# Kernel optimization log

Measured on AMD Instinct MI355X. Metric: run time of the kernel, lower is better.

The kernel has to match this reference:

```python
import jax, jax.numpy as jnp
import numpy as np

N_NODES = 50000
N_EDGES = 1600000
IN_DIM = 128
OUT_DIM = 128
NEG_SLOPE = 0.01  # torch F.leaky_relu default


def setup_inputs() -> dict:
    key = jax.random.key(0)
    ks = jax.random.split(key, 8)
    feat = jax.random.normal(ks[0], (N_NODES, IN_DIM), dtype=jnp.float32)
    src = jax.random.randint(ks[1], (N_EDGES,), 0, N_NODES, dtype=jnp.int32)
    dst = jax.random.randint(ks[2], (N_EDGES,), 0, N_NODES, dtype=jnp.int32)
    W = jax.random.normal(ks[3], (IN_DIM, OUT_DIM), dtype=jnp.float32) / np.sqrt(IN_DIM)
    b = jax.random.normal(ks[4], (OUT_DIM,), dtype=jnp.float32) * 0.01
    attn_w = jax.random.normal(ks[5], (2 * OUT_DIM, 1), dtype=jnp.float32) / np.sqrt(2 * OUT_DIM)
    attn_b = jax.random.normal(ks[6], (1,), dtype=jnp.float32) * 0.01
    mask_weights = jnp.ones((IN_DIM,), dtype=jnp.float32)
    return {"feat": feat, "src": src, "dst": dst, "W": W, "b": b,
            "attn_w": attn_w, "attn_b": attn_b, "mask_weights": mask_weights}


def reference(feat, src, dst, W, b, attn_w, attn_b, mask_weights):
    N = feat.shape[0]
    d = W.shape[1]
    # feature masking + linear projection: [N, out_dim]
    h = (feat * jax.nn.sigmoid(mask_weights)) @ W + b
    # edge scores: attn_mlp(cat([h_src, h_dst])) split into two GEMVs to avoid
    # materializing the [E, 2d] concat
    s_src = (h @ attn_w[:d]).squeeze(-1)   # [N]
    s_dst = (h @ attn_w[d:]).squeeze(-1)   # [N]
    score = s_src[src] + s_dst[dst] + attn_b[0]          # [E]
    score = jnp.where(score >= 0, score, NEG_SLOPE * score)  # leaky_relu
    # segment softmax grouped by destination node (dgl.softmax over in-edges)
    mx = jax.ops.segment_max(score, dst, num_segments=N)     # [N]
    mx = jnp.where(jnp.isfinite(mx), mx, 0.0)                 # nodes w/o edges
    ex = jnp.exp(score - mx[dst])                             # [E]
    denom = jax.ops.segment_sum(ex, dst, num_segments=N)     # [N]
    a = ex / jnp.where(denom == 0, 1.0, denom)[dst]           # [E]
    # weighted scatter-sum: h_new[v] = sum_{(u,v) in E} a_uv * h[u]
    h_new = jax.ops.segment_sum(h[src] * a[:, None], dst, num_segments=N)
    return h_new
```

## Files before the change

kernel.cpp:

```cpp
#include <hip/hip_runtime.h>
#include <hip/hip_fp16.h>
#include <math.h>

#define N_NODES 50000
#define N_EDGES 1600000
#define NB 2000
#define NPB 25
#define NCH 100
#define EPC 16000
#define CAPC 32
#define CAP_LDS 1280
#define CAP_STG 1080
#define RCAP 96
#define SPLIT 8
#define BPS (NB / SPLIT)
#define PLACE_BLOCKS (NCH * SPLIT)
#define PROJ_BLOCKS ((N_NODES + 31) / 32)
#define NBG 5
#define NGRP (NBG * NPB)
#define GQ_BLOCKS ((NB / (NBG * 2)) * 8)

typedef _Float16 f16x8 __attribute__((ext_vector_type(8)));
typedef float f32x4 __attribute__((ext_vector_type(4)));


__global__ __launch_bounds__(256) void k_prep(const float* __restrict__ W,
                                              const float* __restrict__ b,
                                              const float* __restrict__ attn_w,
                                              __half* __restrict__ w16q,
                                              float* __restrict__ waSD,
                                              float* __restrict__ cst) {
    const int blk = blockIdx.x, t = threadIdx.x;
    if (blk < 8) {
        const int k = blk * 16 + (t >> 4), sub = t & 15;
        const float4* W4 = (const float4*)W;
        float4 w0 = W4[k * 32 + sub * 2];
        float4 w1 = W4[k * 32 + sub * 2 + 1];
        const int j0 = sub * 8;
        float pS = w0.x * attn_w[j0]     + w0.y * attn_w[j0 + 1]
                 + w0.z * attn_w[j0 + 2] + w0.w * attn_w[j0 + 3]
                 + w1.x * attn_w[j0 + 4] + w1.y * attn_w[j0 + 5]
                 + w1.z * attn_w[j0 + 6] + w1.w * attn_w[j0 + 7];
        float pD = w0.x * attn_w[128 + j0]     + w0.y * attn_w[128 + j0 + 1]
                 + w0.z * attn_w[128 + j0 + 2] + w0.w * attn_w[128 + j0 + 3]
                 + w1.x * attn_w[128 + j0 + 4] + w1.y * attn_w[128 + j0 + 5]
                 + w1.z * attn_w[128 + j0 + 6] + w1.w * attn_w[128 + j0 + 7];
        pS += __shfl_down(pS, 8); pS += __shfl_down(pS, 4);
        pS += __shfl_down(pS, 2); pS += __shfl_down(pS, 1);
        pD += __shfl_down(pD, 8); pD += __shfl_down(pD, 4);
        pD += __shfl_down(pD, 2); pD += __shfl_down(pD, 1);
        if (sub == 0) { waSD[k] = pS; waSD[128 + k] = pD; }
    } else if (blk < 40) {
        for (int e = (blk - 8) * 256 + t; e < 16384; e += 8192) {
            int j = e & 7, l = (e >> 3) & 63, kb = (e >> 9) & 3, ct = e >> 11;
            int k = kb * 32 + (l >> 4) * 8 + j;
            int c = ct * 16 + (l & 15);
            w16q[e] = __float2half(W[k * 128 + c]);
        }
    } else if (t < 64) {
        float vS = b[t] * attn_w[t]       + b[t + 64] * attn_w[t + 64];
        float vD = b[t] * attn_w[128 + t] + b[t + 64] * attn_w[192 + t];
        for (int off = 32; off; off >>= 1) {
            vS += __shfl_down(vS, off);
            vD += __shfl_down(vD, off);
        }
        if (t == 0) { cst[0] = vS; cst[1] = vD; }
    }
}

__global__ __launch_bounds__(512) void k_fusedA(const float* __restrict__ feat,
                                                const float* __restrict__ b,
                                                const float* __restrict__ mask,
                                                const int* __restrict__ src,
                                                const int* __restrict__ dst,
                                                __half* __restrict__ h16q,
                                                float* __restrict__ s_src,
                                                float* __restrict__ s_dst,
                                                int* __restrict__ cnt,
                                                unsigned* __restrict__ gep,
                                                const __half* __restrict__ w16q,
                                                const float* __restrict__ waSD,
                                                const float* __restrict__ cst) {
    __shared__ __align__(16) char smem[33024];
    const int blk = blockIdx.x;
    const int t = threadIdx.x;

    if (blk < PLACE_BLOCKS) {
        int* cur = (int*)smem;
        unsigned* lcell = (unsigned*)(smem + 1024);
        const int c = blk >> 3, sp = blk & 7;
        const int b0 = sp * BPS;
        for (int i = t; i < BPS; i += 512) cur[i] = 0;
        __syncthreads();
        const int q0 = c * (EPC / 4);
        for (int q = t; q < EPC / 4; q += 512) {
            int4 s4 = ((const int4*)src)[q0 + q];
            int4 d4 = ((const int4*)dst)[q0 + q];
            int ss[4] = {s4.x, s4.y, s4.z, s4.w};
            int dd[4] = {d4.x, d4.y, d4.z, d4.w};
#pragma unroll
            for (int k = 0; k < 4; k++) {
                int d = dd[k];
                int bkt = d / NPB;
                if (bkt >= b0 && bkt < b0 + BPS) {
                    int dl = d - bkt * NPB;
                    int lb = bkt - b0;
                    int r = atomicAdd(&cur[lb], 1);
                    if (r < CAPC)
                        lcell[lb * CAPC + r] = ((unsigned)ss[k] << 5) | (unsigned)dl;
                }
            }
        }
        __syncthreads();
        const uint4* lc4 = (const uint4*)lcell;
        uint4* gp4 = (uint4*)gep;
        for (int idx = t; idx < BPS * (CAPC / 4); idx += 512) {
            int i = idx >> 3, q = idx & 7;
            gp4[((size_t)(b0 + i) * NCH + c) * 8 + q] = lc4[idx];
        }
        for (int i = t; i < BPS; i += 512)
            cnt[(b0 + i) * NCH + c] = min(cur[i], CAPC);
    } else {
        float* sAW = (float*)(smem + 8192);
        float* sAD = (float*)(smem + 8704);
        float* sig = (float*)(smem + 9216);
        const int bb = blk - PLACE_BLOCKS;
        const int row0 = bb * 32;
        if (t < 128) {
            sig[t] = 1.f / (1.f + expf(-mask[t]));
            sAW[t] = waSD[t];
            sAD[t] = waSD[128 + t];
        }
        __syncthreads();
        for (int idx = t; idx < 32 * 32; idx += 512) {
            int r = idx >> 5, c4 = idx & 31;
            int grow = row0 + r;
            float4 f;
            if (grow < N_NODES) f = ((const float4*)feat)[grow * 32 + c4];
            else f = make_float4(0.f, 0.f, 0.f, 0.f);
            int c = c4 * 4;
            ushort4 pk;
            pk.x = __half_as_ushort(__float2half(f.x * sig[c]));
            pk.y = __half_as_ushort(__float2half(f.y * sig[c + 1]));
            pk.z = __half_as_ushort(__float2half(f.z * sig[c + 2]));
            pk.w = __half_as_ushort(__float2half(f.w * sig[c + 3]));
            int byte = (r * 256 + c4 * 8) ^ ((r & 7) << 4);
            *(ushort4*)(smem + byte) = pk;
        }
        __syncthreads();
        const int wv = t >> 6, l = t & 63;
        const int lr = l & 15, lk = l >> 4;
        const f16x8* wq = (const f16x8*)w16q;
        f32x4 acc0 = {0.f, 0.f, 0.f, 0.f};
        f32x4 acc1 = {0.f, 0.f, 0.f, 0.f};
#pragma unroll
        for (int kb = 0; kb < 4; kb++) {
            f16x8 Bf = wq[(wv * 4 + kb) * 64 + l];
            int co = kb * 64 + lk * 16;
            f16x8 A0 = *(const f16x8*)(smem + ((lr * 256 + co) ^ ((lr & 7) << 4)));
            f16x8 A1 = *(const f16x8*)(smem + (((16 + lr) * 256 + co) ^ ((lr & 7) << 4)));
            acc0 = __builtin_amdgcn_mfma_f32_16x16x32_f16(A0, Bf, acc0, 0, 0, 0);
            acc1 = __builtin_amdgcn_mfma_f32_16x16x32_f16(A1, Bf, acc1, 0, 0, 0);
        }
        {
            const int r2 = t >> 4, sub = t & 15;
            f16x8 xv = *(const f16x8*)(smem + ((r2 * 256 + sub * 16) ^ ((r2 & 7) << 4)));
            float ss = 0.f, sd = 0.f;
#pragma unroll
            for (int q = 0; q < 8; q++) {
                float v = (float)xv[q];
                int jj = sub * 8 + q;
                ss = fmaf(v, sAW[jj], ss);
                sd = fmaf(v, sAD[jj], sd);
            }
            ss += __shfl_down(ss, 8); ss += __shfl_down(ss, 4);
            ss += __shfl_down(ss, 2); ss += __shfl_down(ss, 1);
            sd += __shfl_down(sd, 8); sd += __shfl_down(sd, 4);
            sd += __shfl_down(sd, 2); sd += __shfl_down(sd, 1);
            int grow = row0 + r2;
            if (sub == 0 && grow < N_NODES) {
                s_src[grow] = ss + cst[0];
                s_dst[grow] = sd + cst[1];
            }
        }
        const float bj = b[wv * 16 + lr];
        __half* hp = h16q + (size_t)(wv >> 1) * (N_NODES * 32) + ((wv & 1) * 16 + lr);
#pragma unroll
        for (int reg = 0; reg < 4; reg++) {
            int n0 = row0 + lk * 4 + reg;
            if (n0 < N_NODES) hp[(size_t)n0 * 32] = __float2half(acc0[reg] + bj);
            int n1 = n0 + 16;
            if (n1 < N_NODES) hp[(size_t)n1 * 32] = __float2half(acc1[reg] + bj);
        }
    }
}

__global__ __launch_bounds__(256) void k_sort(const float* __restrict__ s_src,
                                              const float* __restrict__ s_dst,
                                              const float* __restrict__ attn_b,
                                              const int* __restrict__ cnt,
                                              unsigned* gep,
                                              int* __restrict__ rp_g) {
    __shared__ unsigned raw[CAP_STG];
    __shared__ unsigned srt[CAP_LDS];
    __shared__ float wbuf[CAP_LDS];
    __shared__ int ccnt[NCH];
    __shared__ int coff[NCH];
    __shared__ int hist[NPB];
    __shared__ int rp[NPB + 1];
    __shared__ float sdl[NPB];
    __shared__ float dinv[NPB];
    __shared__ int totsh;
    const int bkt = blockIdx.x;
    const int t = threadIdx.x;
    if (t < NCH) ccnt[t] = cnt[bkt * NCH + t];
    if (t < NPB) { hist[t] = 0; sdl[t] = s_dst[bkt * NPB + t]; }
    __syncthreads();
    if (t < 64) {
        int i0 = 2 * t, i1 = 2 * t + 1;
        int a0 = (i0 < NCH) ? ccnt[i0] : 0;
        int a1 = (i1 < NCH) ? ccnt[i1] : 0;
        int s = a0 + a1, incl = s;
#pragma unroll
        for (int off = 1; off < 64; off <<= 1) {
            int v = __shfl_up(incl, off);
            if (t >= off) incl += v;
        }
        int excl = incl - s;
        if (i0 < NCH) coff[i0] = excl;
        if (i1 < NCH) coff[i1] = excl + a0;
        if (t == 63) totsh = incl;
    }
    __syncthreads();
    int total = totsh;
    if (total > CAP_STG) total = CAP_STG;
    unsigned* gb = gep + (size_t)bkt * (NCH * CAPC);
    for (int i = t; i < NCH * CAPC; i += 256) {
        unsigned e = gb[i];
        int cell = i >> 5, slot = i & 31;
        if (slot < ccnt[cell]) {
            int pos = coff[cell] + slot;
            if (pos < CAP_STG) {
                int r = atomicAdd(&hist[e & 31], 1);
                raw[pos] = ((unsigned)r << 21) | e;
            }
        }
    }
    __syncthreads();
    if (t < 64) {
        int h = (t < NPB) ? min(hist[t], RCAP) : 0;
        int incl = h;
#pragma unroll
        for (int off = 1; off < 32; off <<= 1) {
            int v = __shfl_up(incl, off);
            if (t >= off) incl += v;
        }
        if (t < NPB) rp[t] = incl - h;
        if (t == NPB - 1) rp[NPB] = incl;
    }
    __syncthreads();
    const float ab = attn_b[0];
    {
        unsigned ev[5];
        float ssv[5];
#pragma unroll
        for (int k = 0; k < 5; k++) {
            int i = t + k * 256;
            ev[k] = (i < total) ? raw[i] : 0xFFFFFFFFu;
        }
#pragma unroll
        for (int k = 0; k < 5; k++)
            ssv[k] = s_src[(ev[k] != 0xFFFFFFFFu) ? (int)((ev[k] >> 5) & 0xFFFFu) : 0];
#pragma unroll
        for (int k = 0; k < 5; k++) {
            if (ev[k] != 0xFFFFFFFFu) {
                unsigned e = ev[k];
                int dl = (int)(e & 31);
                int r = (int)((e >> 21) & 0x7FF);
                if (r < RCAP) {
                    int pos = rp[dl] + r;
                    float sc = ssv[k] + sdl[dl] + ab;
                    sc = sc >= 0.f ? sc : 0.01f * sc;
                    float w = __expf(sc);
                    srt[pos] = (((e >> 5) & 0xFFFFu) << 16) | (unsigned)dl;
                    wbuf[pos] = w;
                }
            }
        }
    }
    __syncthreads();
    if (t < NPB * 8) {
        const int n = t >> 3, sub = t & 7;
        const int lo = rp[n], hi = rp[n + 1];
        float s = 0.f;
        for (int i = lo + sub; i < hi; i += 8) s += wbuf[i];
        s += __shfl_down(s, 4); s += __shfl_down(s, 2); s += __shfl_down(s, 1);
        if (sub == 0) dinv[n] = s > 0.f ? 1.f / s : 0.f;
    }
    __syncthreads();
    const int totp = rp[NPB];
    for (int i = t; i < totp; i += 256) {
        unsigned e = srt[i];
        float a = wbuf[i] * dinv[e & 31];
        gb[i] = (e & 0xFFFF0000u) | (unsigned)__half_as_ushort(__float2half(a));
    }
    if (t <= NPB) rp_g[bkt * 32 + t] = rp[t];
}

__device__ __forceinline__ void accum8(float4& A, float4& B, uint4 u, unsigned e) {
    float w = __half2float(__ushort_as_half((unsigned short)(e & 0xFFFFu)));
    __half2 p0 = *(const __half2*)&u.x;
    __half2 p1 = *(const __half2*)&u.y;
    __half2 p2 = *(const __half2*)&u.z;
    __half2 p3 = *(const __half2*)&u.w;
    float2 f0 = __half22float2(p0), f1 = __half22float2(p1);
    float2 f2 = __half22float2(p2), f3 = __half22float2(p3);
    A.x = fmaf(w, f0.x, A.x); A.y = fmaf(w, f0.y, A.y);
    A.z = fmaf(w, f1.x, A.z); A.w = fmaf(w, f1.y, A.w);
    B.x = fmaf(w, f2.x, B.x); B.y = fmaf(w, f2.y, B.y);
    B.z = fmaf(w, f3.x, B.z); B.w = fmaf(w, f3.y, B.w);
}

__global__ __launch_bounds__(512) void k_gather(const __half* __restrict__ h16q,
                                                const unsigned* __restrict__ gep,
                                                const int* __restrict__ rp_g,
                                                float* __restrict__ out) {
    __shared__ unsigned se[NBG * CAP_LDS];
    __shared__ int rp[NBG * 32];
    const int blk = blockIdx.x;
    const int x = blk & 7;
    const int qq = x & 3;
    const int bg = ((blk >> 3) << 1) + (x >> 2);
    const int bkt0 = bg * NBG;
    const int t = threadIdx.x;
    if (t < NBG * 32 && (t & 31) <= NPB)
        rp[t] = rp_g[(bkt0 + (t >> 5)) * 32 + (t & 31)];
    __syncthreads();
#pragma unroll
    for (int b = 0; b < NBG; b++) {
        const unsigned* gb = gep + (size_t)(bkt0 + b) * (NCH * CAPC);
        const int tot = rp[b * 32 + NPB];
        for (int i = t; i < tot; i += 512) se[b * CAP_LDS + i] = gb[i];
    }
    __syncthreads();
    const int g = t >> 2, dp = t & 3;
    if (g < NGRP) {
        const int b = g / NPB, n = g - b * NPB;
        const int lo = rp[b * 32 + n], hi = rp[b * 32 + n + 1];
        const unsigned* seb = se + b * CAP_LDS;
        const uint4* hq = (const uint4*)h16q + (size_t)qq * (N_NODES * 4) + dp;
        float4 A = {0.f, 0.f, 0.f, 0.f}, B = {0.f, 0.f, 0.f, 0.f};
        for (int i = lo; i < hi; i += 4) {
            unsigned e0 = seb[i];
            unsigned e1 = (i + 1 < hi) ? seb[i + 1] : 0u;
            unsigned e2 = (i + 2 < hi) ? seb[i + 2] : 0u;
            unsigned e3 = (i + 3 < hi) ? seb[i + 3] : 0u;
            uint4 u0 = hq[(e0 >> 16) * 4];
            uint4 u1 = hq[(e1 >> 16) * 4];
            uint4 u2 = hq[(e2 >> 16) * 4];
            uint4 u3 = hq[(e3 >> 16) * 4];
            accum8(A, B, u0, e0);
            accum8(A, B, u1, e1);
            accum8(A, B, u2, e2);
            accum8(A, B, u3, e3);
        }
        float4* o = (float4*)(out + (size_t)(bg * 125 + g) * 128 + qq * 32 + dp * 8);
        o[0] = A;
        o[1] = B;
    }
}

extern "C" void kernel_launch(void* const* d_in, const int* in_sizes, int n_in,
                              void* d_out, int out_size, void* d_ws, size_t ws_size,
                              hipStream_t stream) {
    const float* feat   = (const float*)d_in[0];
    const int*   src    = (const int*)d_in[1];
    const int*   dst    = (const int*)d_in[2];
    const float* W      = (const float*)d_in[3];
    const float* b      = (const float*)d_in[4];
    const float* attn_w = (const float*)d_in[5];
    const float* attn_b = (const float*)d_in[6];
    const float* mask   = (const float*)d_in[7];
    float* out = (float*)d_out;

    char* ws = (char*)d_ws;
    __half*   h16q  = (__half*)(ws + 0);
    float*    s_src = (float*)(ws + 12800000);
    float*    s_dst = (float*)(ws + 13000000);
    int*      cnt   = (int*)(ws + 13200000);
    unsigned* gep   = (unsigned*)(ws + 14000000);
    int*      rp_g  = (int*)(ws + 39600000);
    __half*   w16q  = (__half*)(ws + 39856000);
    float*    waSD  = (float*)(ws + 39888768);
    float*    cst   = (float*)(ws + 39889792);

    k_prep<<<41, 256, 0, stream>>>(W, b, attn_w, w16q, waSD, cst);
    k_fusedA<<<PLACE_BLOCKS + PROJ_BLOCKS, 512, 0, stream>>>(
        feat, b, mask, src, dst, h16q, s_src, s_dst, cnt, gep, w16q, waSD, cst);
    k_sort<<<NB, 256, 0, stream>>>(s_src, s_dst, attn_b, cnt, gep, rp_g);
    k_gather<<<GQ_BLOCKS, 512, 0, stream>>>(h16q, gep, rp_g, out);
}
```

Baseline: 173.3 us.

## Compact edge placement via global atomic bucket counters instead of padded chunk cells

Placement blocks now reserve space in each destination bucket with a global atomicAdd per bucket and write only the valid edges contiguously into a compact per-bucket array. Before, they wrote fixed 32-slot cells per chunk, and the sort kernel had to read all 3200 padded slots and prefix-sum the chunk counts. This cuts global write and read traffic for the edge buffer and simplifies the sort kernel. Block indexing is also remapped so that blocks handling different chunks run together, which spreads contention on the atomics. The cost is global atomic traffic, nondeterministic edge order within a bucket, and an extra pass in k_prep to zero the counters.

```diff
diff --git a/kernel.cpp b/kernel.cpp
--- a/kernel.cpp
+++ b/kernel.cpp
@@ -9,12 +9,12 @@
 #define NCH 100
 #define EPC 16000
 #define CAPC 32
-#define CAP_LDS 1280
 #define CAP_STG 1080
+#define GEPS 1088
 #define RCAP 96
 #define SPLIT 8
 #define BPS (NB / SPLIT)
-#define PLACE_BLOCKS (NCH * SPLIT)
+#define PLACE_EXT 832
 #define PROJ_BLOCKS ((N_NODES + 31) / 32)
 #define NBG 5
 #define NGRP (NBG * NPB)
@@ -29,7 +29,8 @@
                                               const float* __restrict__ attn_w,
                                               __half* __restrict__ w16q,
                                               float* __restrict__ waSD,
-                                              float* __restrict__ cst) {
+                                              float* __restrict__ cst,
+                                              int* __restrict__ gcnt) {
     const int blk = blockIdx.x, t = threadIdx.x;
     if (blk < 8) {
         const int k = blk * 16 + (t >> 4), sub = t & 15;
@@ -57,14 +58,19 @@
             int c = ct * 16 + (l & 15);
             w16q[e] = __float2half(W[k * 128 + c]);
         }
-    } else if (t < 64) {
-        float vS = b[t] * attn_w[t]       + b[t + 64] * attn_w[t + 64];
-        float vD = b[t] * attn_w[128 + t] + b[t + 64] * attn_w[192 + t];
-        for (int off = 32; off; off >>= 1) {
-            vS += __shfl_down(vS, off);
-            vD += __shfl_down(vD, off);
-        }
-        if (t == 0) { cst[0] = vS; cst[1] = vD; }
+    } else if (blk == 40) {
+        if (t < 64) {
+            float vS = b[t] * attn_w[t]       + b[t + 64] * attn_w[t + 64];
+            float vD = b[t] * attn_w[128 + t] + b[t + 64] * attn_w[192 + t];
+            for (int off = 32; off; off >>= 1) {
+                vS += __shfl_down(vS, off);
+                vD += __shfl_down(vD, off);
+            }
+            if (t == 0) { cst[0] = vS; cst[1] = vD; }
+        }
+    } else {
+        int i = (blk - 41) * 256 + t;
+        if (i < NB) gcnt[i] = 0;
     }
 }
 
@@ -76,19 +82,22 @@
                                                 __half* __restrict__ h16q,
                                                 float* __restrict__ s_src,
                                                 float* __restrict__ s_dst,
-                                                int* __restrict__ cnt,
+                                                int* __restrict__ gcnt,
                                                 unsigned* __restrict__ gep,
                                                 const __half* __restrict__ w16q,
                                                 const float* __restrict__ waSD,
                                                 const float* __restrict__ cst) {
-    __shared__ __align__(16) char smem[33024];
+    __shared__ __align__(16) char smem[34048];
     const int blk = blockIdx.x;
     const int t = threadIdx.x;
 
-    if (blk < PLACE_BLOCKS) {
+    if (blk < PLACE_EXT) {
+        const int sp = (blk >> 3) & 7;
+        const int c = ((blk >> 6) << 3) | (blk & 7);
+        if (c >= NCH) return;
         int* cur = (int*)smem;
         unsigned* lcell = (unsigned*)(smem + 1024);
-        const int c = blk >> 3, sp = blk & 7;
+        int* lbase = (int*)(smem + 33024);
         const int b0 = sp * BPS;
         for (int i = t; i < BPS; i += 512) cur[i] = 0;
         __syncthreads();
@@ -112,19 +121,25 @@
             }
         }
         __syncthreads();
-        const uint4* lc4 = (const uint4*)lcell;
-        uint4* gp4 = (uint4*)gep;
-        for (int idx = t; idx < BPS * (CAPC / 4); idx += 512) {
-            int i = idx >> 3, q = idx & 7;
-            gp4[((size_t)(b0 + i) * NCH + c) * 8 + q] = lc4[idx];
-        }
-        for (int i = t; i < BPS; i += 512)
-            cnt[(b0 + i) * NCH + c] = min(cur[i], CAPC);
+        for (int i = t; i < BPS; i += 512) {
+            int n = min(cur[i], CAPC);
+            cur[i] = n;
+            lbase[i] = atomicAdd(&gcnt[b0 + i], n);
+        }
+        __syncthreads();
+        for (int idx = t; idx < BPS * CAPC; idx += 512) {
+            int i = idx >> 5, slot = idx & 31;
+            if (slot < cur[i]) {
+                int pos = lbase[i] + slot;
+                if (pos < CAP_STG)
+                    gep[(size_t)(b0 + i) * GEPS + pos] = lcell[idx];
+            }
+        }
     } else {
         float* sAW = (float*)(smem + 8192);
         float* sAD = (float*)(smem + 8704);
         float* sig = (float*)(smem + 9216);
-        const int bb = blk - PLACE_BLOCKS;
+        const int bb = blk - PLACE_EXT;
         const int row0 = bb * 32;
         if (t < 128) {
             sig[t] = 1.f / (1.f + expf(-mask[t]));
@@ -198,53 +213,26 @@
 __global__ __launch_bounds__(256) void k_sort(const float* __restrict__ s_src,
                                               const float* __restrict__ s_dst,
                                               const float* __restrict__ attn_b,
-                                              const int* __restrict__ cnt,
+                                              const int* __restrict__ gcnt,
                                               unsigned* gep,
                                               int* __restrict__ rp_g) {
     __shared__ unsigned raw[CAP_STG];
-    __shared__ unsigned srt[CAP_LDS];
-    __shared__ float wbuf[CAP_LDS];
-    __shared__ int ccnt[NCH];
-    __shared__ int coff[NCH];
+    __shared__ unsigned srt[CAP_STG];
+    __shared__ float wbuf[CAP_STG];
     __shared__ int hist[NPB];
     __shared__ int rp[NPB + 1];
     __shared__ float sdl[NPB];
     __shared__ float dinv[NPB];
-    __shared__ int totsh;
     const int bkt = blockIdx.x;
     const int t = threadIdx.x;
-    if (t < NCH) ccnt[t] = cnt[bkt * NCH + t];
     if (t < NPB) { hist[t] = 0; sdl[t] = s_dst[bkt * NPB + t]; }
-    __syncthreads();
-    if (t < 64) {
-        int i0 = 2 * t, i1 = 2 * t + 1;
-        int a0 = (i0 < NCH) ? ccnt[i0] : 0;
-        int a1 = (i1 < NCH) ? ccnt[i1] : 0;
-        int s = a0 + a1, incl = s;
-#pragma unroll
-        for (int off = 1; off < 64; off <<= 1) {
-            int v = __shfl_up(incl, off);
-            if (t >= off) incl += v;
-        }
-        int excl = incl - s;
-        if (i0 < NCH) coff[i0] = excl;
-        if (i1 < NCH) coff[i1] = excl + a0;
-        if (t == 63) totsh = incl;
-    }
-    __syncthreads();
-    int total = totsh;
-    if (total > CAP_STG) total = CAP_STG;
-    unsigned* gb = gep + (size_t)bkt * (NCH * CAPC);
-    for (int i = t; i < NCH * CAPC; i += 256) {
+    const int tot = min(gcnt[bkt], CAP_STG);
+    __syncthreads();
+    unsigned* gb = gep + (size_t)bkt * GEPS;
+    for (int i = t; i < tot; i += 256) {
         unsigned e = gb[i];
-        int cell = i >> 5, slot = i & 31;
-        if (slot < ccnt[cell]) {
-            int pos = coff[cell] + slot;
-            if (pos < CAP_STG) {
-                int r = atomicAdd(&hist[e & 31], 1);
-                raw[pos] = ((unsigned)r << 21) | e;
-            }
-        }
+        int r = atomicAdd(&hist[e & 31], 1);
+        raw[i] = ((unsigned)r << 21) | e;
     }
     __syncthreads();
     if (t < 64) {
@@ -266,7 +254,7 @@
 #pragma unroll
         for (int k = 0; k < 5; k++) {
             int i = t + k * 256;
-            ev[k] = (i < total) ? raw[i] : 0xFFFFFFFFu;
+            ev[k] = (i < tot) ? raw[i] : 0xFFFFFFFFu;
         }
 #pragma unroll
         for (int k = 0; k < 5; k++)
@@ -325,7 +313,7 @@
                                                 const unsigned* __restrict__ gep,
                                                 const int* __restrict__ rp_g,
                                                 float* __restrict__ out) {
-    __shared__ unsigned se[NBG * CAP_LDS];
+    __shared__ unsigned se[NBG * GEPS];
     __shared__ int rp[NBG * 32];
     const int blk = blockIdx.x;
     const int x = blk & 7;
@@ -338,16 +326,16 @@
     __syncthreads();
 #pragma unroll
     for (int b = 0; b < NBG; b++) {
-        const unsigned* gb = gep + (size_t)(bkt0 + b) * (NCH * CAPC);
+        const unsigned* gb = gep + (size_t)(bkt0 + b) * GEPS;
         const int tot = rp[b * 32 + NPB];
-        for (int i = t; i < tot; i += 512) se[b * CAP_LDS + i] = gb[i];
+        for (int i = t; i < tot; i += 512) se[b * GEPS + i] = gb[i];
     }
     __syncthreads();
     const int g = t >> 2, dp = t & 3;
     if (g < NGRP) {
         const int b = g / NPB, n = g - b * NPB;
         const int lo = rp[b * 32 + n], hi = rp[b * 32 + n + 1];
-        const unsigned* seb = se + b * CAP_LDS;
+        const unsigned* seb = se + b * GEPS;
         const uint4* hq = (const uint4*)h16q + (size_t)qq * (N_NODES * 4) + dp;
         float4 A = {0.f, 0.f, 0.f, 0.f}, B = {0.f, 0.f, 0.f, 0.f};
         for (int i = lo; i < hi; i += 4) {
@@ -387,16 +375,16 @@
     __half*   h16q  = (__half*)(ws + 0);
     float*    s_src = (float*)(ws + 12800000);
     float*    s_dst = (float*)(ws + 13000000);
-    int*      cnt   = (int*)(ws + 13200000);
-    unsigned* gep   = (unsigned*)(ws + 14000000);
-    int*      rp_g  = (int*)(ws + 39600000);
-    __half*   w16q  = (__half*)(ws + 39856000);
-    float*    waSD  = (float*)(ws + 39888768);
-    float*    cst   = (float*)(ws + 39889792);
-
-    k_prep<<<41, 256, 0, stream>>>(W, b, attn_w, w16q, waSD, cst);
-    k_fusedA<<<PLACE_BLOCKS + PROJ_BLOCKS, 512, 0, stream>>>(
-        feat, b, mask, src, dst, h16q, s_src, s_dst, cnt, gep, w16q, waSD, cst);
-    k_sort<<<NB, 256, 0, stream>>>(s_src, s_dst, attn_b, cnt, gep, rp_g);
+    int*      gcnt  = (int*)(ws + 13200000);
+    unsigned* gep   = (unsigned*)(ws + 13300000);
+    int*      rp_g  = (int*)(ws + 22100000);
+    __half*   w16q  = (__half*)(ws + 22400000);
+    float*    waSD  = (float*)(ws + 22440000);
+    float*    cst   = (float*)(ws + 22442000);
+
+    k_prep<<<49, 256, 0, stream>>>(W, b, attn_w, w16q, waSD, cst, gcnt);
+    k_fusedA<<<PLACE_EXT + PROJ_BLOCKS, 512, 0, stream>>>(
+        feat, b, mask, src, dst, h16q, s_src, s_dst, gcnt, gep, w16q, waSD, cst);
+    k_sort<<<NB, 256, 0, stream>>>(s_src, s_dst, attn_b, gcnt, gep, rp_g);
     k_gather<<<GQ_BLOCKS, 512, 0, stream>>>(h16q, gep, rp_g, out);
 }
```

Result: faster. 163.7 us (-5.5%).
